# Kernel optimization log

Hardware: AMD Instinct MI355X
Metric: run time of the kernel (lower is better)

The kernel has to match this reference:

```python
import jax, jax.numpy as jnp
import numpy as np

B, T, E, H = 4, 2048, 1024, 16
HD = E // H  # head_dim = 64


def setup_inputs() -> dict:
    key = jax.random.key(0)
    ks = jax.random.split(key, 6)
    s_in = 1.0 / np.sqrt(HD)
    s_e = 1.0 / np.sqrt(E)
    return {
        "x": jax.random.normal(ks[0], (B, T, E), dtype=jnp.float32),
        # per-head qkv linear: weight [H, HD, 3*HD], bias [H, 3*HD]
        "W_qkv": jax.random.uniform(ks[1], (H, HD, 3 * HD), dtype=jnp.float32, minval=-s_in, maxval=s_in),
        "b_qkv": jax.random.uniform(ks[2], (H, 3 * HD), dtype=jnp.float32, minval=-s_in, maxval=s_in),
        # output projection [E, E]
        "W_proj": jax.random.uniform(ks[3], (E, E), dtype=jnp.float32, minval=-s_e, maxval=s_e),
        "b_proj": jax.random.uniform(ks[4], (E,), dtype=jnp.float32, minval=-s_e, maxval=s_e),
    }


def reference(x, W_qkv, b_qkv, W_proj, b_proj):
    b, t, e = x.shape
    h, hd = W_qkv.shape[0], W_qkv.shape[1]
    # Each head consumes its own contiguous slice of the channel dim.
    xh = x.reshape(b, t, h, hd)  # [B,T,H,HD]
    qkv = jnp.einsum("bthd,hde->bthe", xh, W_qkv) + b_qkv  # [B,T,H,3*HD]
    q, k, v = jnp.split(qkv, 3, axis=-1)  # each [B,T,H,HD]
    scale = 1.0 / (hd ** 0.5 + 1e-05)  # matches (embed_dim ** 0.5 + 1e-05) with embed_dim=head_dim
    attn = jnp.einsum("bthd,bshd->bhts", q, k) * scale  # [B,H,T,T]
    causal = jnp.tril(jnp.ones((t, t), dtype=bool))
    attn = jnp.where(causal, attn, -jnp.inf)
    attn = jax.nn.softmax(attn, axis=-1)
    out = jnp.einsum("bhts,bshd->bthd", attn, v).reshape(b, t, e)  # concat heads
    # dropout is identity in eval mode
    return out @ W_proj.T + b_proj
```

## Files before the change

### kernel.cpp

```cpp
#include <hip/hip_runtime.h>
#include <hip/hip_bf16.h>

#define B_ 4
#define T_ 2048
#define E_ 1024
#define H_ 16
#define HD_ 64

typedef __attribute__((ext_vector_type(8))) short bf16x8;
typedef __attribute__((ext_vector_type(4))) float f32x4;
typedef __attribute__((ext_vector_type(16))) float f32x16;

__device__ inline ushort f2b(float f) {
  union { __hip_bfloat16 h; ushort u; } c;
  c.h = __float2bfloat16(f);
  return c.u;
}
__device__ inline short f2bs(float f) {
  union { __hip_bfloat16 h; short s; } c;
  c.h = __float2bfloat16(f);
  return c.s;
}
__device__ inline int cvtpk(float lo, float hi) {
  int r;
  asm("v_cvt_pk_bf16_f32 %0, %1, %2" : "=v"(r) : "v"(lo), "v"(hi));
  return r;
}
__device__ inline f32x16 zero16() {
  f32x16 z;
#pragma unroll
  for (int i = 0; i < 16; ++i) z[i] = 0.0f;
  return z;
}

__device__ inline void gload16(const ushort* gsrc, ushort* lds_uniform_base) {
  __builtin_amdgcn_global_load_lds(
      (const __attribute__((address_space(1))) void*)gsrc,
      (__attribute__((address_space(3))) void*)lds_uniform_base, 16, 0, 0);
}

__global__ __launch_bounds__(256) void cvt_kernel(const float* __restrict__ Wq,
                                                  ushort* __restrict__ Wt,
                                                  const float* __restrict__ Wp,
                                                  ushort* __restrict__ Wb) {
  int bid = blockIdx.x;
  if (bid < 768) {
    int gtid = bid * 256 + threadIdx.x;
    int h = gtid / (HD_ * 192);
    int rem = gtid % (HD_ * 192);
    int d = rem / 192;
    int e = rem % 192;
    int v = (e >> 6) * 64 + (e & 3) * 16 + ((e >> 2) & 15);
    Wt[h * (192 * HD_) + v * HD_ + d] = f2b(Wq[gtid]);
  } else {
    int i = ((bid - 768) * 256 + threadIdx.x) * 4;
    int n = i >> 10;
    int c = i & 1023;
    int vn = (n & ~63) + (n & 3) * 16 + ((n >> 2) & 15);
    float4 f = *reinterpret_cast<const float4*>(Wp + i);
    ushort4 u;
    u.x = f2b(f.x); u.y = f2b(f.y); u.z = f2b(f.z); u.w = f2b(f.w);
    *reinterpret_cast<ushort4*>(Wb + (size_t)vn * E_ + c) = u;
  }
}

__global__ __launch_bounds__(256) void qkv_kernel(const float* __restrict__ x,
                                                  const ushort* __restrict__ Wt,
                                                  const float* __restrict__ bq,
                                                  ushort* __restrict__ Q,
                                                  ushort* __restrict__ K,
                                                  ushort* __restrict__ Vt) {
  const float SCALE = (1.0f / (8.0f + 1e-5f)) * 1.4426950408889634f;
  int wave = threadIdx.x >> 6, lane = threadIdx.x & 63;
  int lo = lane & 15, hi = lane >> 4;
  int bh = blockIdx.y, b = bh >> 4, h = bh & 15;
  int t0 = blockIdx.x * 64 + wave * 16;

  const float* xr = x + (size_t)(b * T_ + t0 + lo) * E_ + h * HD_;
  bf16x8 af[2];
#pragma unroll
  for (int c = 0; c < 2; ++c) {
    float4 f0 = *reinterpret_cast<const float4*>(xr + c * 32 + hi * 8);
    float4 f1 = *reinterpret_cast<const float4*>(xr + c * 32 + hi * 8 + 4);
    bf16x8 v;
    v[0] = f2bs(f0.x); v[1] = f2bs(f0.y); v[2] = f2bs(f0.z); v[3] = f2bs(f0.w);
    v[4] = f2bs(f1.x); v[5] = f2bs(f1.y); v[6] = f2bs(f1.z); v[7] = f2bs(f1.w);
    af[c] = v;
  }

  const ushort* Wh = Wt + h * (192 * HD_);
#pragma unroll
  for (int g = 0; g < 3; ++g) {
    f32x4 accg[4];
#pragma unroll
    for (int j = 0; j < 4; ++j) {
      int n0 = (g * 4 + j) * 16;
      bf16x8 bf0 = *reinterpret_cast<const bf16x8*>(Wh + (size_t)(n0 + lo) * HD_ + hi * 8);
      bf16x8 bf1 = *reinterpret_cast<const bf16x8*>(Wh + (size_t)(n0 + lo) * HD_ + 32 + hi * 8);
      f32x4 acc = {0.0f, 0.0f, 0.0f, 0.0f};
      acc = __builtin_amdgcn_mfma_f32_16x16x32_bf16(af[0], bf0, acc, 0, 0, 0);
      acc = __builtin_amdgcn_mfma_f32_16x16x32_bf16(af[1], bf1, acc, 0, 0, 0);
      accg[j] = acc;
    }
    float4 bq4 = *reinterpret_cast<const float4*>(bq + h * 192 + g * 64 + 4 * lo);
    if (g < 2) {
      ushort* dst = (g == 0) ? Q : K;
      float sc = (g == 0) ? SCALE : 1.0f;
#pragma unroll
      for (int r = 0; r < 4; ++r) {
        int t = t0 + hi * 4 + r;
        ushort4 u;
        u.x = f2b((accg[0][r] + bq4.x) * sc);
        u.y = f2b((accg[1][r] + bq4.y) * sc);
        u.z = f2b((accg[2][r] + bq4.z) * sc);
        u.w = f2b((accg[3][r] + bq4.w) * sc);
        *reinterpret_cast<ushort4*>(dst + ((size_t)bh * T_ + t) * HD_ + 4 * lo) = u;
      }
    } else {
      float bj[4] = {bq4.x, bq4.y, bq4.z, bq4.w};
#pragma unroll
      for (int j = 0; j < 4; ++j) {
        int hd = 4 * lo + j;
        ushort4 u;
        u.x = f2b(accg[j][0] + bj[j]);
        u.y = f2b(accg[j][1] + bj[j]);
        u.z = f2b(accg[j][2] + bj[j]);
        u.w = f2b(accg[j][3] + bj[j]);
        int col = t0 + hi * 4 + hd * 8;
        col &= (T_ - 1);
        *reinterpret_cast<ushort4*>(Vt + ((size_t)bh * HD_ + hd) * T_ + col) = u;
      }
    }
  }
}

__global__ __launch_bounds__(512) void attn_kernel(const ushort* __restrict__ Q,
                                                   const ushort* __restrict__ K,
                                                   const ushort* __restrict__ Vt,
                                                   ushort* __restrict__ AO) {
  __shared__ ushort Ks[4][64 * 64];
  __shared__ ushort Vs[4][64 * 64];

  int wave = threadIdx.x >> 6, lane = threadIdx.x & 63;
  int q5 = lane & 31, hi5 = lane >> 5;
  int bh = blockIdx.x, b = bh >> 4, h = bh & 15;
  int y = blockIdx.y;
  int qt = (y < 4) ? (7 - y) : (y - 4);
  int qw = qt * 256 + wave * 32;

  const ushort* Kbh = K + (size_t)bh * T_ * HD_;
  const ushort* Vbh = Vt + (size_t)bh * HD_ * T_;

  bf16x8 qf[4];
#pragma unroll
  for (int ks = 0; ks < 4; ++ks)
    qf[ks] = *reinterpret_cast<const bf16x8*>(
        Q + ((size_t)bh * T_ + qw + q5) * HD_ + ks * 16 + hi5 * 8);

  f32x16 ot[2];
  ot[0] = zero16(); ot[1] = zero16();
  float mreg = -1e30f, lreg = 0.0f;

  int srow = lane >> 3;
  int sch = lane & 7;

  int ntiles = qt * 4 + 4;

#define STAGE(BUF, TILE)                                                        \
  {                                                                             \
    int kt_ = (TILE) << 6;                                                      \
    int row = wave * 8 + srow;                                                  \
    const ushort* gk = Kbh + (size_t)(kt_ + row) * HD_ + ((sch ^ (row & 7)) * 8); \
    gload16(gk, &Ks[BUF][(wave * 8) * 64]);                                     \
    int col = (kt_ + ((sch ^ (row & 7)) + row) * 8) & (T_ - 1);                 \
    const ushort* gv = Vbh + (size_t)row * T_ + col;                            \
    gload16(gv, &Vs[BUF][(wave * 8) * 64]);                                     \
  }

  auto compute_tile = [&](int tile, int buf) {
    int kt = tile << 6;
    if (kt > qw + 31) return;
    f32x16 s[2];
#pragma unroll
    for (int g = 0; g < 2; ++g) {
      int krow = g * 32 + q5;
      bf16x8 kf[4];
#pragma unroll
      for (int ks = 0; ks < 4; ++ks)
        kf[ks] = *reinterpret_cast<const bf16x8*>(
            &Ks[buf][krow * 64 + (((2 * ks + hi5) ^ (krow & 7)) * 8)]);
      f32x16 acc = zero16();
      __builtin_amdgcn_s_setprio(1);
#pragma unroll
      for (int ks = 0; ks < 4; ++ks)
        acc = __builtin_amdgcn_mfma_f32_32x32x16_bf16(kf[ks], qf[ks], acc, 0, 0, 0);
      __builtin_amdgcn_s_setprio(0);
      s[g] = acc;
    }
    if (kt + 63 > qw) {
      int q = qw + q5;
#pragma unroll
      for (int g = 0; g < 2; ++g)
#pragma unroll
        for (int r = 0; r < 16; ++r) {
          int key = kt + g * 32 + (r & 3) + 8 * (r >> 2) + 4 * hi5;
          if (key > q) s[g][r] = -1e30f;
        }
    }
    float t8[8];
#pragma unroll
    for (int i = 0; i < 8; ++i)
      t8[i] = fmaxf(fmaxf(s[0][i], s[0][i + 8]), fmaxf(s[1][i], s[1][i + 8]));
    float mx = fmaxf(fmaxf(fmaxf(t8[0], t8[1]), fmaxf(t8[2], t8[3])),
                     fmaxf(fmaxf(t8[4], t8[5]), fmaxf(t8[6], t8[7])));
    mx = fmaxf(mx, __shfl_xor(mx, 32));
    float nm = fmaxf(mreg, mx);
    float alpha = exp2f(mreg - nm);
    mreg = nm;
#pragma unroll
    for (int g = 0; g < 2; ++g)
#pragma unroll
      for (int r = 0; r < 16; ++r)
        s[g][r] = exp2f(s[g][r] - nm);
    float u8[8];
#pragma unroll
    for (int i = 0; i < 8; ++i)
      u8[i] = (s[0][i] + s[0][i + 8]) + (s[1][i] + s[1][i + 8]);
    float rs = ((u8[0] + u8[1]) + (u8[2] + u8[3])) + ((u8[4] + u8[5]) + (u8[6] + u8[7]));
    rs += __shfl_xor(rs, 32);
    lreg = lreg * alpha + rs;
#pragma unroll
    for (int nh = 0; nh < 2; ++nh)
#pragma unroll
      for (int r = 0; r < 16; ++r) ot[nh][r] *= alpha;

    bf16x8 pb4[4];
#pragma unroll
    for (int ks = 0; ks < 4; ++ks) {
      int g = ks >> 1;
      int R0 = 2 * (ks & 1), R1 = R0 + 1;
      int a0w0 = cvtpk(s[g][4 * R0 + 0], s[g][4 * R0 + 1]);
      int a0w1 = cvtpk(s[g][4 * R0 + 2], s[g][4 * R0 + 3]);
      int a1w0 = cvtpk(s[g][4 * R1 + 0], s[g][4 * R1 + 1]);
      int a1w1 = cvtpk(s[g][4 * R1 + 2], s[g][4 * R1 + 3]);
      int pA0w0 = __shfl_xor(a0w0, 32);
      int pA0w1 = __shfl_xor(a0w1, 32);
      int pA1w0 = __shfl_xor(a1w0, 32);
      int pA1w1 = __shfl_xor(a1w1, 32);
      int4 w;
      w.x = hi5 ? pA1w0 : a0w0;
      w.y = hi5 ? pA1w1 : a0w1;
      w.z = hi5 ? a1w0 : pA0w0;
      w.w = hi5 ? a1w1 : pA0w1;
      pb4[ks] = *reinterpret_cast<bf16x8*>(&w);
    }
#pragma unroll
    for (int nh = 0; nh < 2; ++nh) {
      int vrow = nh * 32 + q5;
      bf16x8 vf[4];
#pragma unroll
      for (int ks = 0; ks < 4; ++ks)
        vf[ks] = *reinterpret_cast<const bf16x8*>(
            &Vs[buf][vrow * 64 + (((2 * ks + hi5) ^ (vrow & 7)) * 8)]);
      __builtin_amdgcn_s_setprio(1);
#pragma unroll
      for (int ks = 0; ks < 4; ++ks)
        ot[nh] = __builtin_amdgcn_mfma_f32_32x32x16_bf16(vf[ks], pb4[ks], ot[nh], 0, 0, 0);
      __builtin_amdgcn_s_setprio(0);
    }
  };

  STAGE(0, 0);
  STAGE(1, 1);

  int npairs = ntiles >> 1;
  for (int p = 0; p < npairs; ++p) {
    int t0 = 2 * p, t1 = 2 * p + 1;
    asm volatile("s_waitcnt vmcnt(0)" ::: "memory");
    __builtin_amdgcn_s_barrier();
    {
      int pr0 = t0 + 2, pr1 = t0 + 3;
      int s0 = (pr0 < ntiles) ? pr0 : 0;
      int s1 = (pr1 < ntiles) ? pr1 : 0;
      STAGE(pr0 & 3, s0);
      STAGE(pr1 & 3, s1);
    }
    compute_tile(t0, t0 & 3);
    compute_tile(t1, t1 & 3);
  }
#undef STAGE

  float inv = 1.0f / lreg;
  int t = qw + q5;
  ushort* aop = AO + ((size_t)(b * T_ + t) * H_ + h) * HD_;
#pragma unroll
  for (int nh = 0; nh < 2; ++nh)
#pragma unroll
    for (int R = 0; R < 4; ++R) {
      ushort4 u;
      u.x = f2b(ot[nh][4 * R + 0] * inv);
      u.y = f2b(ot[nh][4 * R + 1] * inv);
      u.z = f2b(ot[nh][4 * R + 2] * inv);
      u.w = f2b(ot[nh][4 * R + 3] * inv);
      *reinterpret_cast<ushort4*>(aop + nh * 32 + 8 * R + 4 * hi5) = u;
    }
}

__global__ __launch_bounds__(256) void proj_kernel(const ushort* __restrict__ A,
                                                   const ushort* __restrict__ Wb,
                                                   const float* __restrict__ bias,
                                                   float* __restrict__ out) {
  __shared__ ushort As[2][128 * 32];
  __shared__ ushort Bs[2][128 * 32];
  int tid = threadIdx.x;
  int wave = tid >> 6, lane = tid & 63;
  int lo = lane & 15, hi = lane >> 4;
  int wr = wave >> 1, wc = wave & 1;
  int m0 = blockIdx.y * 128, n0 = blockIdx.x * 128;

  int srow4 = lane >> 2;
  int sch4 = lane & 3;
  int swz = sch4 ^ ((srow4 >> 1) & 3);

#define PSTAGE(BUF, K0)                                                          \
  {                                                                              \
    _Pragma("unroll")                                                            \
    for (int rep = 0; rep < 2; ++rep) {                                          \
      int row = wave * 32 + rep * 16 + srow4;                                    \
      gload16(A + (size_t)(m0 + row) * E_ + (K0) + swz * 8,                      \
              &As[BUF][(wave * 32 + rep * 16) * 32]);                            \
      gload16(Wb + (size_t)(n0 + row) * E_ + (K0) + swz * 8,                     \
              &Bs[BUF][(wave * 32 + rep * 16) * 32]);                            \
    }                                                                            \
  }

  f32x4 acc[4][4] = {};
  PSTAGE(0, 0);
  asm volatile("s_waitcnt vmcnt(0)" ::: "memory");
  __syncthreads();

  int cur = 0;
  for (int k0 = 0; k0 < E_; k0 += 32) {
    int kpre = (k0 + 32) & (E_ - 1);
    PSTAGE(cur ^ 1, kpre);
    bf16x8 af[4], bfr[4];
#pragma unroll
    for (int i = 0; i < 4; ++i) {
      int row = wr * 64 + i * 16 + lo;
      af[i] = *reinterpret_cast<const bf16x8*>(
          &As[cur][row * 32 + ((hi ^ ((row >> 1) & 3)) * 8)]);
    }
#pragma unroll
    for (int j = 0; j < 4; ++j) {
      int row = wc * 64 + j * 16 + lo;
      bfr[j] = *reinterpret_cast<const bf16x8*>(
          &Bs[cur][row * 32 + ((hi ^ ((row >> 1) & 3)) * 8)]);
    }
    __builtin_amdgcn_s_setprio(1);
#pragma unroll
    for (int i = 0; i < 4; ++i)
#pragma unroll
      for (int j = 0; j < 4; ++j)
        acc[i][j] = __builtin_amdgcn_mfma_f32_16x16x32_bf16(af[i], bfr[j], acc[i][j], 0, 0, 0);
    __builtin_amdgcn_s_setprio(0);
    asm volatile("s_waitcnt vmcnt(0)" ::: "memory");
    __syncthreads();
    cur ^= 1;
  }
#undef PSTAGE

  float4 b4 = *reinterpret_cast<const float4*>(bias + n0 + wc * 64 + 4 * lo);
#pragma unroll
  for (int i = 0; i < 4; ++i)
#pragma unroll
    for (int r = 0; r < 4; ++r) {
      int mm = m0 + wr * 64 + i * 16 + hi * 4 + r;
      float4 u;
      u.x = acc[i][0][r] + b4.x;
      u.y = acc[i][1][r] + b4.y;
      u.z = acc[i][2][r] + b4.z;
      u.w = acc[i][3][r] + b4.w;
      *reinterpret_cast<float4*>(out + (size_t)mm * E_ + n0 + wc * 64 + 4 * lo) = u;
    }
}

extern "C" void kernel_launch(void* const* d_in, const int* in_sizes, int n_in,
                              void* d_out, int out_size, void* d_ws, size_t ws_size,
                              hipStream_t stream) {
  (void)in_sizes; (void)n_in; (void)out_size; (void)ws_size;
  const float* x  = (const float*)d_in[0];
  const float* Wq = (const float*)d_in[1];
  const float* bq = (const float*)d_in[2];
  const float* Wp = (const float*)d_in[3];
  const float* bp = (const float*)d_in[4];
  float* out = (float*)d_out;

  const size_t NQ = (size_t)B_ * H_ * T_ * HD_;
  ushort* ws = (ushort*)d_ws;
  ushort* Q  = ws;
  ushort* K  = ws + NQ;
  ushort* Vt = ws + 2 * NQ;
  ushort* AO = ws + 3 * NQ;
  ushort* Wb = ws + 4 * NQ;
  ushort* Wt = ws + 4 * NQ + (size_t)E_ * E_;

  cvt_kernel<<<dim3(1792), dim3(256), 0, stream>>>(Wq, Wt, Wp, Wb);
  qkv_kernel<<<dim3(T_ / 64, B_ * H_), dim3(256), 0, stream>>>(x, Wt, bq, Q, K, Vt);
  attn_kernel<<<dim3(B_ * H_, 8), dim3(512), 0, stream>>>(Q, K, Vt, AO);
  proj_kernel<<<dim3(E_ / 128, (B_ * T_) / 128), dim3(256), 0, stream>>>(AO, Wb, bp, out);
}
```

Measured before the change: 145.1 us.

## Split attention key range across two blocks and merge partials

Adds a split-K attention path. Each query tile now gets two blocks, one processing even key tiles and one processing odd key tiles, which doubles the grid from 512 to 1024 blocks to improve occupancy and load balance across CUs. Each block writes unnormalized bf16 partial outputs plus row max and sum, and a new combine kernel merges them into the attention output. This costs an extra launch, extra global traffic for the partials, and an additional bf16 rounding of the unnormalized partials. The path is used only when the workspace is large enough, otherwise the original kernel runs.

```diff
diff --git a/kernel.cpp b/kernel.cpp
--- a/kernel.cpp
+++ b/kernel.cpp
@@ -20,6 +20,9 @@
   union { __hip_bfloat16 h; short s; } c;
   c.h = __float2bfloat16(f);
   return c.s;
+}
+__device__ inline float b2f(ushort u) {
+  return __uint_as_float(((unsigned)u) << 16);
 }
 __device__ inline int cvtpk(float lo, float hi) {
   int r;
@@ -134,22 +137,39 @@
   }
 }
 
-__global__ __launch_bounds__(512) void attn_kernel(const ushort* __restrict__ Q,
-                                                   const ushort* __restrict__ K,
-                                                   const ushort* __restrict__ Vt,
-                                                   ushort* __restrict__ AO) {
+#define ATTN_PREAMBLE()                                                         \
+  int wave = threadIdx.x >> 6, lane = threadIdx.x & 63;                         \
+  int q5 = lane & 31, hi5 = lane >> 5;                                          \
+  int bh = blockIdx.x, b = bh >> 4, h = bh & 15;                                \
+  const ushort* Kbh = K + (size_t)bh * T_ * HD_;                                \
+  const ushort* Vbh = Vt + (size_t)bh * HD_ * T_;                               \
+  int srow = lane >> 3;                                                         \
+  int sch = lane & 7;
+
+#define ATTN_STAGE_BODY(BUF, KT_)                                               \
+  {                                                                             \
+    int row = wave * 8 + srow;                                                  \
+    const ushort* gk = Kbh + (size_t)((KT_) + row) * HD_ + ((sch ^ (row & 7)) * 8); \
+    gload16(gk, &Ks[BUF][(wave * 8) * 64]);                                     \
+    int col = ((KT_) + ((sch ^ (row & 7)) + row) * 8) & (T_ - 1);               \
+    const ushort* gv = Vbh + (size_t)row * T_ + col;                            \
+    gload16(gv, &Vs[BUF][(wave * 8) * 64]);                                     \
+  }
+
+__global__ __launch_bounds__(512) void attn_split_kernel(const ushort* __restrict__ Q,
+                                                         const ushort* __restrict__ K,
+                                                         const ushort* __restrict__ Vt,
+                                                         ushort* __restrict__ O0,
+                                                         ushort* __restrict__ O1,
+                                                         float* __restrict__ mlf) {
   __shared__ ushort Ks[4][64 * 64];
   __shared__ ushort Vs[4][64 * 64];
 
-  int wave = threadIdx.x >> 6, lane = threadIdx.x & 63;
-  int q5 = lane & 31, hi5 = lane >> 5;
-  int bh = blockIdx.x, b = bh >> 4, h = bh & 15;
+  ATTN_PREAMBLE();
   int y = blockIdx.y;
-  int qt = (y < 4) ? (7 - y) : (y - 4);
+  int y2 = y >> 1, half = y & 1;
+  int qt = (y2 < 4) ? (7 - y2) : (y2 - 4);
   int qw = qt * 256 + wave * 32;
-
-  const ushort* Kbh = K + (size_t)bh * T_ * HD_;
-  const ushort* Vbh = Vt + (size_t)bh * HD_ * T_;
 
   bf16x8 qf[4];
 #pragma unroll
@@ -161,24 +181,12 @@
   ot[0] = zero16(); ot[1] = zero16();
   float mreg = -1e30f, lreg = 0.0f;
 
-  int srow = lane >> 3;
-  int sch = lane & 7;
-
-  int ntiles = qt * 4 + 4;
-
-#define STAGE(BUF, TILE)                                                        \
-  {                                                                             \
-    int kt_ = (TILE) << 6;                                                      \
-    int row = wave * 8 + srow;                                                  \
-    const ushort* gk = Kbh + (size_t)(kt_ + row) * HD_ + ((sch ^ (row & 7)) * 8); \
-    gload16(gk, &Ks[BUF][(wave * 8) * 64]);                                     \
-    int col = (kt_ + ((sch ^ (row & 7)) + row) * 8) & (T_ - 1);                 \
-    const ushort* gv = Vbh + (size_t)row * T_ + col;                            \
-    gload16(gv, &Vs[BUF][(wave * 8) * 64]);                                     \
-  }
-
-  auto compute_tile = [&](int tile, int buf) {
-    int kt = tile << 6;
+  int nlist = 2 * qt + 2;
+
+#define SSTAGE(BUF, LI)  { int kt_ = (half + 2 * (LI)) << 6; ATTN_STAGE_BODY(BUF, kt_) }
+
+  auto compute_tile = [&](int li, int buf) {
+    int kt = (half + 2 * li) << 6;
     if (kt > qw + 31) return;
     f32x16 s[2];
 #pragma unroll
@@ -270,8 +278,194 @@
     }
   };
 
-  STAGE(0, 0);
-  STAGE(1, 1);
+  SSTAGE(0, 0);
+  SSTAGE(1, 1);
+
+  int npairs = nlist >> 1;
+  for (int p = 0; p < npairs; ++p) {
+    int l0 = 2 * p, l1 = 2 * p + 1;
+    asm volatile("s_waitcnt vmcnt(0)" ::: "memory");
+    __builtin_amdgcn_s_barrier();
+    {
+      int pr0 = l0 + 2, pr1 = l0 + 3;
+      int s0 = (pr0 < nlist) ? pr0 : 0;
+      int s1 = (pr1 < nlist) ? pr1 : 0;
+      SSTAGE(pr0 & 3, s0);
+      SSTAGE(pr1 & 3, s1);
+    }
+    compute_tile(l0, l0 & 3);
+    compute_tile(l1, l1 & 3);
+  }
+#undef SSTAGE
+
+  ushort* Opart = half ? O1 : O0;
+  int t = qw + q5;
+  ushort* aop = Opart + ((size_t)(b * T_ + t) * H_ + h) * HD_;
+#pragma unroll
+  for (int nh = 0; nh < 2; ++nh)
+#pragma unroll
+    for (int R = 0; R < 4; ++R) {
+      ushort4 u;
+      u.x = f2b(ot[nh][4 * R + 0]);
+      u.y = f2b(ot[nh][4 * R + 1]);
+      u.z = f2b(ot[nh][4 * R + 2]);
+      u.w = f2b(ot[nh][4 * R + 3]);
+      *reinterpret_cast<ushort4*>(aop + nh * 32 + 8 * R + 4 * hi5) = u;
+    }
+  if (hi5 == 0) {
+    size_t mlrow = (size_t)bh * T_ + qw + q5;
+    float2 v = {mreg, lreg};
+    *reinterpret_cast<float2*>(mlf + ((size_t)half * (B_ * H_ * T_) + mlrow) * 2) = v;
+  }
+}
+
+__global__ __launch_bounds__(256) void combine_kernel(const ushort* __restrict__ O0,
+                                                      const ushort* __restrict__ O1,
+                                                      const float* __restrict__ mlf,
+                                                      ushort* __restrict__ AO) {
+  int gid = blockIdx.x * 256 + threadIdx.x;
+  int row = gid >> 3;
+  int c8 = (gid & 7) * 8;
+  int h = row & 15;
+  int bt = row >> 4;
+  int t = bt & (T_ - 1);
+  int b = bt >> 11;
+  size_t mlrow = ((size_t)(b * H_ + h) * T_ + t);
+  float2 ml0 = *reinterpret_cast<const float2*>(mlf + mlrow * 2);
+  float2 ml1 = *reinterpret_cast<const float2*>(mlf + ((size_t)(B_ * H_ * T_) + mlrow) * 2);
+  float m = fmaxf(ml0.x, ml1.x);
+  float w0 = exp2f(ml0.x - m), w1 = exp2f(ml1.x - m);
+  float inv = 1.0f / (ml0.y * w0 + ml1.y * w1);
+  const bf16x8 a = *reinterpret_cast<const bf16x8*>(O0 + (size_t)row * HD_ + c8);
+  const bf16x8 c = *reinterpret_cast<const bf16x8*>(O1 + (size_t)row * HD_ + c8);
+  bf16x8 o;
+#pragma unroll
+  for (int j = 0; j < 8; ++j)
+    o[j] = f2bs((b2f((ushort)a[j]) * w0 + b2f((ushort)c[j]) * w1) * inv);
+  *reinterpret_cast<bf16x8*>(AO + (size_t)row * HD_ + c8) = o;
+}
+
+__global__ __launch_bounds__(512) void attn_kernel(const ushort* __restrict__ Q,
+                                                   const ushort* __restrict__ K,
+                                                   const ushort* __restrict__ Vt,
+                                                   ushort* __restrict__ AO) {
+  __shared__ ushort Ks[4][64 * 64];
+  __shared__ ushort Vs[4][64 * 64];
+
+  ATTN_PREAMBLE();
+  int y = blockIdx.y;
+  int qt = (y < 4) ? (7 - y) : (y - 4);
+  int qw = qt * 256 + wave * 32;
+
+  bf16x8 qf[4];
+#pragma unroll
+  for (int ks = 0; ks < 4; ++ks)
+    qf[ks] = *reinterpret_cast<const bf16x8*>(
+        Q + ((size_t)bh * T_ + qw + q5) * HD_ + ks * 16 + hi5 * 8);
+
+  f32x16 ot[2];
+  ot[0] = zero16(); ot[1] = zero16();
+  float mreg = -1e30f, lreg = 0.0f;
+
+  int ntiles = qt * 4 + 4;
+
+#define FSTAGE(BUF, TILE)  { int kt_ = (TILE) << 6; ATTN_STAGE_BODY(BUF, kt_) }
+
+  auto compute_tile = [&](int tile, int buf) {
+    int kt = tile << 6;
+    if (kt > qw + 31) return;
+    f32x16 s[2];
+#pragma unroll
+    for (int g = 0; g < 2; ++g) {
+      int krow = g * 32 + q5;
+      bf16x8 kf[4];
+#pragma unroll
+      for (int ks = 0; ks < 4; ++ks)
+        kf[ks] = *reinterpret_cast<const bf16x8*>(
+            &Ks[buf][krow * 64 + (((2 * ks + hi5) ^ (krow & 7)) * 8)]);
+      f32x16 acc = zero16();
+      __builtin_amdgcn_s_setprio(1);
+#pragma unroll
+      for (int ks = 0; ks < 4; ++ks)
+        acc = __builtin_amdgcn_mfma_f32_32x32x16_bf16(kf[ks], qf[ks], acc, 0, 0, 0);
+      __builtin_amdgcn_s_setprio(0);
+      s[g] = acc;
+    }
+    if (kt + 63 > qw) {
+      int q = qw + q5;
+#pragma unroll
+      for (int g = 0; g < 2; ++g)
+#pragma unroll
+        for (int r = 0; r < 16; ++r) {
+          int key = kt + g * 32 + (r & 3) + 8 * (r >> 2) + 4 * hi5;
+          if (key > q) s[g][r] = -1e30f;
+        }
+    }
+    float t8[8];
+#pragma unroll
+    for (int i = 0; i < 8; ++i)
+      t8[i] = fmaxf(fmaxf(s[0][i], s[0][i + 8]), fmaxf(s[1][i], s[1][i + 8]));
+    float mx = fmaxf(fmaxf(fmaxf(t8[0], t8[1]), fmaxf(t8[2], t8[3])),
+                     fmaxf(fmaxf(t8[4], t8[5]), fmaxf(t8[6], t8[7])));
+    mx = fmaxf(mx, __shfl_xor(mx, 32));
+    float nm = fmaxf(mreg, mx);
+    float alpha = exp2f(mreg - nm);
+    mreg = nm;
+#pragma unroll
+    for (int g = 0; g < 2; ++g)
+#pragma unroll
+      for (int r = 0; r < 16; ++r)
+        s[g][r] = exp2f(s[g][r] - nm);
+    float u8[8];
+#pragma unroll
+    for (int i = 0; i < 8; ++i)
+      u8[i] = (s[0][i] + s[0][i + 8]) + (s[1][i] + s[1][i + 8]);
+    float rs = ((u8[0] + u8[1]) + (u8[2] + u8[3])) + ((u8[4] + u8[5]) + (u8[6] + u8[7]));
+    rs += __shfl_xor(rs, 32);
+    lreg = lreg * alpha + rs;
+#pragma unroll
+    for (int nh = 0; nh < 2; ++nh)
+#pragma unroll
+      for (int r = 0; r < 16; ++r) ot[nh][r] *= alpha;
+
+    bf16x8 pb4[4];
+#pragma unroll
+    for (int ks = 0; ks < 4; ++ks) {
+      int g = ks >> 1;
+      int R0 = 2 * (ks & 1), R1 = R0 + 1;
+      int a0w0 = cvtpk(s[g][4 * R0 + 0], s[g][4 * R0 + 1]);
+      int a0w1 = cvtpk(s[g][4 * R0 + 2], s[g][4 * R0 + 3]);
+      int a1w0 = cvtpk(s[g][4 * R1 + 0], s[g][4 * R1 + 1]);
+      int a1w1 = cvtpk(s[g][4 * R1 + 2], s[g][4 * R1 + 3]);
+      int pA0w0 = __shfl_xor(a0w0, 32);
+      int pA0w1 = __shfl_xor(a0w1, 32);
+      int pA1w0 = __shfl_xor(a1w0, 32);
+      int pA1w1 = __shfl_xor(a1w1, 32);
+      int4 w;
+      w.x = hi5 ? pA1w0 : a0w0;
+      w.y = hi5 ? pA1w1 : a0w1;
+      w.z = hi5 ? a1w0 : pA0w0;
+      w.w = hi5 ? a1w1 : pA0w1;
+      pb4[ks] = *reinterpret_cast<bf16x8*>(&w);
+    }
+#pragma unroll
+    for (int nh = 0; nh < 2; ++nh) {
+      int vrow = nh * 32 + q5;
+      bf16x8 vf[4];
+#pragma unroll
+      for (int ks = 0; ks < 4; ++ks)
+        vf[ks] = *reinterpret_cast<const bf16x8*>(
+            &Vs[buf][vrow * 64 + (((2 * ks + hi5) ^ (vrow & 7)) * 8)]);
+      __builtin_amdgcn_s_setprio(1);
+#pragma unroll
+      for (int ks = 0; ks < 4; ++ks)
+        ot[nh] = __builtin_amdgcn_mfma_f32_32x32x16_bf16(vf[ks], pb4[ks], ot[nh], 0, 0, 0);
+      __builtin_amdgcn_s_setprio(0);
+    }
+  };
+
+  FSTAGE(0, 0);
+  FSTAGE(1, 1);
 
   int npairs = ntiles >> 1;
   for (int p = 0; p < npairs; ++p) {
@@ -282,13 +476,13 @@
       int pr0 = t0 + 2, pr1 = t0 + 3;
       int s0 = (pr0 < ntiles) ? pr0 : 0;
       int s1 = (pr1 < ntiles) ? pr1 : 0;
-      STAGE(pr0 & 3, s0);
-      STAGE(pr1 & 3, s1);
+      FSTAGE(pr0 & 3, s0);
+      FSTAGE(pr1 & 3, s1);
     }
     compute_tile(t0, t0 & 3);
     compute_tile(t1, t1 & 3);
   }
-#undef STAGE
+#undef FSTAGE
 
   float inv = 1.0f / lreg;
   int t = qw + q5;
@@ -387,7 +581,7 @@
 extern "C" void kernel_launch(void* const* d_in, const int* in_sizes, int n_in,
                               void* d_out, int out_size, void* d_ws, size_t ws_size,
                               hipStream_t stream) {
-  (void)in_sizes; (void)n_in; (void)out_size; (void)ws_size;
+  (void)in_sizes; (void)n_in; (void)out_size;
   const float* x  = (const float*)d_in[0];
   const float* Wq = (const float*)d_in[1];
   const float* bq = (const float*)d_in[2];
@@ -396,16 +590,36 @@
   float* out = (float*)d_out;
 
   const size_t NQ = (size_t)B_ * H_ * T_ * HD_;
+  const size_t WBN = (size_t)E_ * E_;
+  const size_t WTN = (size_t)H_ * 192 * HD_;
+  const size_t MLN = (size_t)2 * B_ * H_ * T_ * 2;
+  size_t need_split = (5 * NQ + WBN + WTN) * 2 + MLN * 4;
+
   ushort* ws = (ushort*)d_ws;
   ushort* Q  = ws;
   ushort* K  = ws + NQ;
   ushort* Vt = ws + 2 * NQ;
-  ushort* AO = ws + 3 * NQ;
-  ushort* Wb = ws + 4 * NQ;
-  ushort* Wt = ws + 4 * NQ + (size_t)E_ * E_;
-
-  cvt_kernel<<<dim3(1792), dim3(256), 0, stream>>>(Wq, Wt, Wp, Wb);
-  qkv_kernel<<<dim3(T_ / 64, B_ * H_), dim3(256), 0, stream>>>(x, Wt, bq, Q, K, Vt);
-  attn_kernel<<<dim3(B_ * H_, 8), dim3(512), 0, stream>>>(Q, K, Vt, AO);
-  proj_kernel<<<dim3(E_ / 128, (B_ * T_) / 128), dim3(256), 0, stream>>>(AO, Wb, bp, out);
-}
+  ushort* O0 = ws + 3 * NQ;
+
+  if (ws_size >= need_split) {
+    ushort* O1 = ws + 4 * NQ;
+    ushort* Wb = ws + 5 * NQ;
+    ushort* Wt = ws + 5 * NQ + WBN;
+    float* mlf = (float*)(ws + 5 * NQ + WBN + WTN);
+
+    cvt_kernel<<<dim3(1792), dim3(256), 0, stream>>>(Wq, Wt, Wp, Wb);
+    qkv_kernel<<<dim3(T_ / 64, B_ * H_), dim3(256), 0, stream>>>(x, Wt, bq, Q, K, Vt);
+    attn_split_kernel<<<dim3(B_ * H_, 16), dim3(512), 0, stream>>>(Q, K, Vt, O0, O1, mlf);
+    combine_kernel<<<dim3((B_ * T_ * H_ * 8) / 256), dim3(256), 0, stream>>>(O0, O1, mlf, Q);
+    proj_kernel<<<dim3(E_ / 128, (B_ * T_) / 128), dim3(256), 0, stream>>>(Q, Wb, bp, out);
+  } else {
+    ushort* AO = ws + 3 * NQ;
+    ushort* Wb = ws + 4 * NQ;
+    ushort* Wt = ws + 4 * NQ + WBN;
+
+    cvt_kernel<<<dim3(1792), dim3(256), 0, stream>>>(Wq, Wt, Wp, Wb);
+    qkv_kernel<<<dim3(T_ / 64, B_ * H_), dim3(256), 0, stream>>>(x, Wt, bq, Q, K, Vt);
+    attn_kernel<<<dim3(B_ * H_, 8), dim3(512), 0, stream>>>(Q, K, Vt, AO);
+    proj_kernel<<<dim3(E_ / 128, (B_ * T_) / 128), dim3(256), 0, stream>>>(AO, Wb, bp, out);
+  }
+}
```

Result: slower. 155.5 us (+7.2%).
